# Kernel tuning notes

Measured on AMD Instinct MI355X. Metric: run time of the kernel, lower is better.

The kernel has to match this reference:

```python
import jax, jax.numpy as jnp
import numpy as np

B, N, H, W, C = 4, 8, 512, 512, 65536
SCALING = 10.0
EPS = 1e-10
ITERS = 17  # 2**17 > C+1, so pointer doubling covers any tree depth


def setup_inputs() -> dict:
    key = jax.random.key(0)
    k = jax.random.split(key, 8)
    # per-component grey-level differences (already in scaled/quantized units)
    diff = jax.random.uniform(k[0], (B, N, C), jnp.float32, 0.0, 4.0)
    # raw 15 attributes: xmin,ymin,xmax,ymax,area,angle,pca_big,pca_small,hu1..7
    bbox = jax.random.uniform(k[1], (B, N, C, 4), jnp.float32, 0.0, 512.0)
    area = 1.0 + jax.random.uniform(k[2], (B, N, C, 1)) * 1e4
    angle = (jax.random.uniform(k[3], (B, N, C, 1)) - 0.5) * np.pi
    pca_big = 1e-3 + jax.random.uniform(k[4], (B, N, C, 1)) * 100.0
    pca_small = pca_big * jax.random.uniform(k[5], (B, N, C, 1))
    hu = jax.random.normal(k[6], (B, N, C, 7)) * 0.01
    attrs = jnp.concatenate([bbox, area, angle, pca_big, pca_small, hu], axis=-1)
    # topologically ordered parent pointers: parent[c] < c; root (c=0) -> sentinel C
    idx = jnp.arange(C, dtype=jnp.float32)
    u = jax.random.uniform(k[7], (B, N, C))
    parent = jnp.floor(u * idx).astype(jnp.int32)
    parent = parent.at[..., 0].set(C)
    pix2cc = jax.random.randint(jax.random.fold_in(key, 1), (B, N, H, W), 0, C, dtype=jnp.int32)
    weight = jax.random.uniform(jax.random.fold_in(key, 2), (N, 17, 1), jnp.float32, -0.01, 0.01)
    bias = jnp.zeros((N, 1), jnp.float32)
    return dict(diff=diff, attrs=attrs, weight=weight, bias=bias, parent=parent, pix2cc=pix2cc)


def _log_scaling(f):
    # faithful port of maxtree _log_scaling: 15 raw attrs -> 17 features
    lshape = jnp.sqrt(f[..., 7:8]) / (jnp.sqrt(f[..., 6:7]) + EPS)
    cosa = jnp.cos(f[..., 5:6])
    sina = jnp.sin(f[..., 5:6])
    area = jnp.log(f[..., 4:5])
    tail = jnp.log(jnp.abs(f[..., 6:]) + EPS) * jnp.sign(f[..., 6:])
    return jnp.concatenate([f[..., :4], area, tail, lshape, cosa, sina], axis=-1)


def reference(diff, attrs, weight, bias, parent, pix2cc):
    feats = _log_scaling(attrs)                                   # (B,N,C,17)
    logits = jnp.einsum('bnck,nko->bnco', feats, weight)[..., 0]  # (B,N,C)
    logits = logits + bias[None, :, :]                            # bias (N,1) broadcasts over C
    scores = jax.nn.sigmoid(logits)                               # per-component keep score
    w = diff * scores                                             # weighted level increment
    # append zero-weight self-loop sentinel so path sums terminate at the root
    wz = jnp.concatenate([w, jnp.zeros((B, N, 1), w.dtype)], axis=-1)
    pz = jnp.concatenate([parent, jnp.full((B, N, 1), C, jnp.int32)], axis=-1)
    s, ptr = wz, pz
    for _ in range(ITERS):  # pointer doubling: s[c] = sum of diff*score along root path
        s = s + jnp.take_along_axis(s, ptr, axis=-1)
        ptr = jnp.take_along_axis(ptr, ptr, axis=-1)
    val = s[..., :C]                                              # (B,N,C) reconstructed levels
    flat = jnp.take_along_axis(val, pix2cc.reshape(B, N, H * W), axis=-1)
    return flat.reshape(B, N, H, W) / SCALING
```

## Files before the change

### kernel.cpp

```cpp
#include <hip/hip_runtime.h>

#define BB 4
#define NN 8
#define HH 512
#define WW 512
#define CC 65536
#define EPSF 1e-10f
#define NF 15
#define NFE 17
#define MLOW 4096

struct WP { float w; int p; };

__global__ __launch_bounds__(256) void k_score(
    const float* __restrict__ diff, const float* __restrict__ attrs,
    const float* __restrict__ weight, const float* __restrict__ bias,
    const int* __restrict__ parent, WP* __restrict__ wp)
{
    __shared__ float sat[256 * NF];
    const int tid = threadIdx.x;
    const long long base = (long long)blockIdx.x * 256;
    const int n = (int)((base / CC) % NN);

    const float4* src = (const float4*)(attrs + base * NF);
    float4* dst4 = (float4*)sat;
    #pragma unroll
    for (int i = 0; i < 4; ++i) {
        int k = tid + i * 256;
        if (k < (256 * NF) / 4) dst4[k] = src[k];
    }
    __syncthreads();

    float f[NF];
    #pragma unroll
    for (int j = 0; j < NF; ++j) f[j] = sat[tid * NF + j];

    float wgt[NFE];
    #pragma unroll
    for (int k = 0; k < NFE; ++k) wgt[k] = weight[n * NFE + k];
    const float bs = bias[n];

    float logit = bs;
    logit += f[0] * wgt[0] + f[1] * wgt[1] + f[2] * wgt[2] + f[3] * wgt[3];
    logit += logf(f[4]) * wgt[4];
    #pragma unroll
    for (int j = 0; j < 9; ++j) {
        float x = f[6 + j];
        float lg = logf(fabsf(x) + EPSF);
        float t = (x > 0.f) ? lg : ((x < 0.f) ? -lg : 0.f);
        logit += t * wgt[5 + j];
    }
    logit += (sqrtf(f[7]) / (sqrtf(f[6]) + EPSF)) * wgt[14];
    logit += cosf(f[5]) * wgt[15];
    logit += sinf(f[5]) * wgt[16];

    const float score = 1.f / (1.f + expf(-logit));
    const long long idx = base + tid;
    WP o;
    o.w = diff[idx] * score;
    o.p = parent[idx];
    wp[idx] = o;
}

__global__ __launch_bounds__(256) void k_low(
    const WP* __restrict__ wp, float* __restrict__ valLow)
{
    __shared__ float sA[MLOW + 1], sB[MLOW + 1];
    __shared__ int   pA[MLOW + 1], pB[MLOW + 1];
    const int tid = threadIdx.x;
    const long long tbase = (long long)blockIdx.x << 16;

    for (int i = tid; i < MLOW; i += 256) {
        WP e = wp[tbase + i];
        sA[i] = e.w;
        pA[i] = (e.p >= MLOW) ? MLOW : e.p;
    }
    if (tid == 0) { sA[MLOW] = 0.f; pA[MLOW] = MLOW; }
    __syncthreads();

    float* scur = sA; float* snxt = sB;
    int*   pcur = pA; int*   pnxt = pB;
    for (int it = 0; it < 12; ++it) {
        for (int i = tid; i <= MLOW; i += 256) {
            int p = pcur[i];
            snxt[i] = scur[i] + scur[p];
            pnxt[i] = pcur[p];
        }
        __syncthreads();
        float* st = scur; scur = snxt; snxt = st;
        int*   pt = pcur; pcur = pnxt; pnxt = pt;
    }
    for (int i = tid; i < MLOW; i += 256)
        valLow[((long long)blockIdx.x << 12) + i] = scur[i];
}

__global__ __launch_bounds__(256) void k_chain(
    const WP* __restrict__ wp, const float* __restrict__ valLow,
    float* __restrict__ val)
{
    const int bid = blockIdx.x;
    const int tree  = ((bid & 7) << 2) + ((bid >> 3) >> 8);
    const int chunk = (bid >> 3) & 255;
    const int node0 = (chunk << 8) + threadIdx.x;
    const long long tbase = (long long)tree << 16;
    const float* vlow = valLow + ((long long)tree << 12);

    float acc;
    if (node0 < MLOW) {
        acc = vlow[node0];
    } else {
        WP cur = wp[tbase + node0];
        acc = cur.w;
        int p = cur.p;
        while (p >= MLOW) {
            WP nx = wp[tbase + p];
            acc += nx.w;
            p = nx.p;
        }
        acc += vlow[p];
    }
    val[tbase + node0] = acc;
}

__global__ __launch_bounds__(256) void k_gather(
    const float* __restrict__ val, const int* __restrict__ pix,
    float* __restrict__ out)
{
    const int bid = blockIdx.x;
    const int tree  = ((bid & 7) << 2) + ((bid >> 3) >> 8);
    const int chunk = (bid >> 3) & 255;
    const long long i4 = ((long long)tree << 18) + ((long long)chunk << 10)
                       + (long long)threadIdx.x * 4;
    const float* v = val + ((long long)tree << 16);
    int4 cc = *(const int4*)(pix + i4);
    float4 o;
    o.x = v[cc.x] * 0.1f;
    o.y = v[cc.y] * 0.1f;
    o.z = v[cc.z] * 0.1f;
    o.w = v[cc.w] * 0.1f;
    *(float4*)(out + i4) = o;
}

extern "C" void kernel_launch(void* const* d_in, const int* in_sizes, int n_in,
                              void* d_out, int out_size, void* d_ws, size_t ws_size,
                              hipStream_t stream) {
    const float* diff   = (const float*)d_in[0];
    const float* attrs  = (const float*)d_in[1];
    const float* weight = (const float*)d_in[2];
    const float* bias   = (const float*)d_in[3];
    const int*   parent = (const int*)d_in[4];
    const int*   pix    = (const int*)d_in[5];
    float* out = (float*)d_out;

    WP*    wp     = (WP*)d_ws;
    float* val    = (float*)((char*)d_ws + (size_t)BB * NN * CC * sizeof(WP));
    float* valLow = (float*)((char*)val  + (size_t)BB * NN * CC * sizeof(float));

    const long long total = (long long)BB * NN * CC;
    const long long tout  = (long long)BB * NN * HH * WW;

    k_score <<<(int)(total / 256), 256, 0, stream>>>(diff, attrs, weight, bias, parent, wp);
    k_low   <<<BB * NN, 256, 0, stream>>>(wp, valLow);
    k_chain <<<(int)(total / 256), 256, 0, stream>>>(wp, valLow, val);
    k_gather<<<(int)(tout / 1024), 256, 0, stream>>>(val, pix, out);
}
```

Baseline: 289.3 us.

## Replace shared-memory pointer doubling with per-node chain walk; nontemporal gather I/O

The low-node kernel no longer runs 12 rounds of pointer doubling inside 32 single blocks. It now launches one thread per low node across many blocks, and each thread walks its parent chain to the root in global memory. This removes the serial, barrier-heavy tail kernel that used only 32 workgroups, at the cost of divergent chain lengths and more global reads. The gather kernel also uses nontemporal loads for the pixel indices and nontemporal stores for the output, so these streams pollute the cache less.

Result: faster. 278.8 us (-3.6%).

```diff
diff --git a/kernel.cpp b/kernel.cpp
--- a/kernel.cpp
+++ b/kernel.cpp
@@ -11,6 +11,9 @@
 #define MLOW 4096
 
 struct WP { float w; int p; };
+
+typedef int   nint4  __attribute__((ext_vector_type(4)));
+typedef float nfloat4 __attribute__((ext_vector_type(4)));
 
 __global__ __launch_bounds__(256) void k_score(
     const float* __restrict__ diff, const float* __restrict__ attrs,
@@ -65,33 +68,19 @@
 __global__ __launch_bounds__(256) void k_low(
     const WP* __restrict__ wp, float* __restrict__ valLow)
 {
-    __shared__ float sA[MLOW + 1], sB[MLOW + 1];
-    __shared__ int   pA[MLOW + 1], pB[MLOW + 1];
-    const int tid = threadIdx.x;
-    const long long tbase = (long long)blockIdx.x << 16;
-
-    for (int i = tid; i < MLOW; i += 256) {
-        WP e = wp[tbase + i];
-        sA[i] = e.w;
-        pA[i] = (e.p >= MLOW) ? MLOW : e.p;
+    const int i = blockIdx.x * 256 + threadIdx.x;
+    const int tree = i >> 12;
+    const int node = i & (MLOW - 1);
+    const long long tbase = (long long)tree << 16;
+    WP cur = wp[tbase + node];
+    float acc = cur.w;
+    int p = cur.p;
+    while (p != CC) {
+        WP nx = wp[tbase + p];
+        acc += nx.w;
+        p = nx.p;
     }
-    if (tid == 0) { sA[MLOW] = 0.f; pA[MLOW] = MLOW; }
-    __syncthreads();
-
-    float* scur = sA; float* snxt = sB;
-    int*   pcur = pA; int*   pnxt = pB;
-    for (int it = 0; it < 12; ++it) {
-        for (int i = tid; i <= MLOW; i += 256) {
-            int p = pcur[i];
-            snxt[i] = scur[i] + scur[p];
-            pnxt[i] = pcur[p];
-        }
-        __syncthreads();
-        float* st = scur; scur = snxt; snxt = st;
-        int*   pt = pcur; pcur = pnxt; pnxt = pt;
-    }
-    for (int i = tid; i < MLOW; i += 256)
-        valLow[((long long)blockIdx.x << 12) + i] = scur[i];
+    valLow[i] = acc;
 }
 
 __global__ __launch_bounds__(256) void k_chain(
@@ -132,13 +121,13 @@
     const long long i4 = ((long long)tree << 18) + ((long long)chunk << 10)
                        + (long long)threadIdx.x * 4;
     const float* v = val + ((long long)tree << 16);
-    int4 cc = *(const int4*)(pix + i4);
-    float4 o;
+    nint4 cc = __builtin_nontemporal_load((const nint4*)(pix + i4));
+    nfloat4 o;
     o.x = v[cc.x] * 0.1f;
     o.y = v[cc.y] * 0.1f;
     o.z = v[cc.z] * 0.1f;
     o.w = v[cc.w] * 0.1f;
-    *(float4*)(out + i4) = o;
+    __builtin_nontemporal_store(o, (nfloat4*)(out + i4));
 }
 
 extern "C" void kernel_launch(void* const* d_in, const int* in_sizes, int n_in,
@@ -160,7 +149,7 @@
     const long long tout  = (long long)BB * NN * HH * WW;
 
     k_score <<<(int)(total / 256), 256, 0, stream>>>(diff, attrs, weight, bias, parent, wp);
-    k_low   <<<BB * NN, 256, 0, stream>>>(wp, valLow);
+    k_low   <<<(BB * NN * MLOW) / 256, 256, 0, stream>>>(wp, valLow);
     k_chain <<<(int)(total / 256), 256, 0, stream>>>(wp, valLow, val);
     k_gather<<<(int)(tout / 1024), 256, 0, stream>>>(val, pix, out);
 }
```
